# Kernel tuning notes

Hardware: AMD Instinct MI355X
Metric: run time of the kernel (lower is better)

## Reference

```python
import jax, jax.numpy as jnp
import numpy as np


def _l2norm(x, eps=1e-6):
    return x / jnp.sqrt(jnp.sum(x * x, axis=-1, keepdims=True) + eps)


def setup_inputs() -> dict:
    key = jax.random.key(0)
    k1, k2, k3, k4 = jax.random.split(key, 4)
    b, h, L, dk, dv = 2, 8, 4096, 128, 128
    q = jax.random.normal(k1, (b, h, L, dk), jnp.float32)
    k = jax.random.normal(k2, (b, h, L, dk), jnp.float32)
    v = jax.random.normal(k3, (b, h, L, dv), jnp.float32)
    beta = jax.random.uniform(k4, (b, h, L), jnp.float32)  # sigmoid(b_proj) in module -> (0,1)
    return {"q": q, "k": k, "v": v, "beta": beta, "chunk_size": 32}


def _delta_rule_chunkwise(q, k, v, beta, chunk_size):
    b, h, L, dk = q.shape
    dv = v.shape[-1]
    c = chunk_size
    pad = (-L) % c
    if pad:
        q = jnp.pad(q, ((0, 0), (0, 0), (0, pad), (0, 0)))
        k = jnp.pad(k, ((0, 0), (0, 0), (0, pad), (0, 0)))
        v = jnp.pad(v, ((0, 0), (0, 0), (0, pad), (0, 0)))
        beta = jnp.pad(beta, ((0, 0), (0, 0), (0, pad)))
    Lp = L + pad
    n = Lp // c

    q = _l2norm(q)
    k = _l2norm(k)
    v = v * beta[..., None]
    kb = k * beta[..., None]

    # (b,h,n,c,d)
    resh = lambda t: t.reshape(b, h, n, c, t.shape[-1])
    q, k, v, kb = resh(q), resh(k), resh(v), resh(kb)

    tri = jnp.triu(jnp.ones((c, c), bool), 0)        # upper incl diag
    tri_s = jnp.triu(jnp.ones((c, c), bool), 1)      # strict upper

    # forward substitution: inv = (I + strictly-lower(k_beta k^T))^{-1}-style recurrence
    inv = -jnp.einsum('bhncd,bhned->bhnce', kb, k)
    inv = jnp.where(tri, 0.0, inv)
    for i in range(1, c):  # fixed small chunk_size loop (c=32)
        upd = jnp.einsum('bhnk,bhnkj->bhnj', inv[..., i, :], inv[..., :, :i])
        inv = inv.at[..., i, :i].add(upd)
    inv = inv + jnp.eye(c, dtype=inv.dtype)

    u = inv @ v    # (b,h,n,c,dv)
    w = inv @ kb   # (b,h,n,c,dk)

    # chunk-recurrent state scan over the n blocks
    qs = jnp.moveaxis(q, 2, 0)
    ks = jnp.moveaxis(k, 2, 0)
    us = jnp.moveaxis(u, 2, 0)
    ws = jnp.moveaxis(w, 2, 0)
    S0 = jnp.zeros((b, h, dk, dv), q.dtype)

    def step(S, blk):
        q_i, k_i, u_i, w_i = blk
        attn = jnp.einsum('bhcd,bhed->bhce', q_i, k_i)
        attn = jnp.where(tri_s, 0.0, attn)                       # causal within chunk
        u_i = u_i - jnp.einsum('bhcd,bhde->bhce', w_i, S)
        o_i = jnp.einsum('bhcd,bhde->bhce', q_i, S) + jnp.einsum('bhce,bhed->bhcd', attn, u_i)
        S = S + jnp.einsum('bhcd,bhce->bhde', k_i, u_i)
        return S, o_i

    S, out = jax.lax.scan(step, S0, (qs, ks, us, ws))
    out = jnp.moveaxis(out, 0, 2).reshape(b, h, Lp, dv)[:, :, :L]
    return out, S


def reference(q, k, v, beta, chunk_size):
    return _delta_rule_chunkwise(q, k, v, beta, int(chunk_size))
```

## Files before the change

kernel.cpp:

```cpp
#include <hip/hip_runtime.h>
#include <cstddef>

#define BH   16
#define LSEQ 4096
#define DK   128
#define DV   128
#define C    32
#define NCH  128
#define DVB  16
#define NDVB 8
#define PP   136
#define PC   40
#define PS   136
#define AP   33

#define RECSZ 22528
#define OQ    0
#define OWH   4096
#define OWL   8192
#define OKTH  12288
#define OKTL  16384
#define OATH  20480
#define OATL  21504

typedef __attribute__((ext_vector_type(4))) float f32x4;
typedef __attribute__((ext_vector_type(8))) short short8;
typedef __attribute__((ext_vector_type(4))) short s16x4;

__device__ inline unsigned split_bf16(float x) {
    unsigned u = __builtin_bit_cast(unsigned, x);
    unsigned r = u + 0x7fffu + ((u >> 16) & 1u);
    unsigned h = r >> 16;
    float hf = __builtin_bit_cast(float, r & 0xffff0000u);
    float res = x - hf;
    unsigned u2 = __builtin_bit_cast(unsigned, res);
    unsigned r2 = u2 + 0x7fffu + ((u2 >> 16) & 1u);
    return (h << 16) | (r2 >> 16);
}
__device__ inline short hi_bf16(float x) {
    unsigned u = __builtin_bit_cast(unsigned, x);
    return (short)((u + 0x7fffu + ((u >> 16) & 1u)) >> 16);
}
__device__ inline short trunc_bf16(float x) {
    return (short)(__builtin_bit_cast(unsigned, x) >> 16);
}

__device__ inline short8 fld(const short* P, int row0, int pitch, int k0, int lane) {
    return *(const short8*)(P + (row0 + (lane & 15)) * pitch + k0 + ((lane >> 4) << 3));
}
__device__ inline short8 fldz128(const short* P, int row0, int ks, int lane) {
    int row = row0 + (lane & 15);
    int c = ks * 4 + (lane >> 4);
    return *(const short8*)(P + row * 128 + ((c ^ (row & 7)) << 3));
}
__device__ inline short8 fldz32(const short* P, int row0, int lane) {
    int row = row0 + (lane & 15);
    int c = lane >> 4;
    return *(const short8*)(P + row * 32 + ((c ^ (row & 3)) << 3));
}
__device__ inline f32x4 mf(short8 a, short8 b, f32x4 c) {
    return __builtin_amdgcn_mfma_f32_16x16x32_bf16(a, b, c, 0, 0, 0);
}
__device__ inline void build_ifrags(int lane, short8& Iev, short8& Iod) {
    int n = lane & 15, q = lane >> 4;
#pragma unroll
    for (int j = 0; j < 8; ++j) {
        Iev[j] = (q * 8 + j == n)      ? (short)0x3F80 : (short)0;
        Iod[j] = (q * 8 + j == n + 16) ? (short)0x3F80 : (short)0;
    }
}
__device__ inline void store8_z128(short* Pg, int row, int col0, s16x4 v) {
    int c = col0 >> 3;
    *(s16x4*)(Pg + row * 128 + ((c ^ (row & 7)) << 3) + (col0 & 7)) = v;
}
__device__ inline void store8_z32(short* Pg, int row, int col0, s16x4 v) {
    int c = col0 >> 3;
    *(s16x4*)(Pg + row * 32 + ((c ^ (row & 3)) << 3) + (col0 & 7)) = v;
}
__device__ inline void dma1k(const short* g, short* l, int lane) {
    __builtin_amdgcn_global_load_lds(
        (const __attribute__((address_space(1))) unsigned int*)(g + lane * 8),
        (__attribute__((address_space(3))) unsigned int*)l, 16, 0, 0);
}
__device__ inline void bar_lgkm() {
    asm volatile("s_waitcnt lgkmcnt(0)" ::: "memory");
    __builtin_amdgcn_s_barrier();
    asm volatile("" ::: "memory");
}

__global__ __launch_bounds__(256) void k_prep(const float* __restrict__ Q,
                                              const float* __restrict__ K,
                                              const float* __restrict__ V,
                                              const float* __restrict__ Beta,
                                              short* __restrict__ RECg,
                                              float* __restrict__ Uws) {
    __shared__ short knh[C * PP], knl[C * PP], vh[C * PP], vl[C * PP], qh[C * PP];
    __shared__ short knTh[DK * PC], knTl[DK * PC], vTh[DK * PC], vTl[DK * PC];
    __shared__ short Th[C * PC], Tl[C * PC];
    __shared__ float A[C * AP];
    __shared__ float sbeta[C];

    const int t = threadIdx.x, lane = t & 63, wv = t >> 6;
    const int quad = (t >> 4) & 3, l15 = t & 15;
    const int g = blockIdx.x;
    const size_t base = (size_t)g * (C * DK);
    short* rec = RECg + (size_t)g * RECSZ;
    short8 Iev, Iod;
    build_ifrags(lane, Iev, Iod);

    if (t < C) sbeta[t] = Beta[(size_t)(g >> 7) * LSEQ + (size_t)(g & 127) * C + t];

    const int sr = t >> 3, sc = (t & 7) * 16;
    f32x4 kk[4], vv[4], qq[4];
#pragma unroll
    for (int g4 = 0; g4 < 4; ++g4) {
        kk[g4] = *(const f32x4*)(K + base + 16 * t + 4 * g4);
        vv[g4] = *(const f32x4*)(V + base + 16 * t + 4 * g4);
        qq[g4] = *(const f32x4*)(Q + base + 16 * t + 4 * g4);
    }
    float ssk = 0.f, ssq = 0.f;
#pragma unroll
    for (int g4 = 0; g4 < 4; ++g4) {
#pragma unroll
        for (int e = 0; e < 4; ++e) {
            ssk += kk[g4][e] * kk[g4][e];
            ssq += qq[g4][e] * qq[g4][e];
        }
    }
    ssk += __shfl_xor(ssk, 1); ssk += __shfl_xor(ssk, 2); ssk += __shfl_xor(ssk, 4);
    ssq += __shfl_xor(ssq, 1); ssq += __shfl_xor(ssq, 2); ssq += __shfl_xor(ssq, 4);
    const float rk = rsqrtf(ssk + 1e-6f), rq = rsqrtf(ssq + 1e-6f);
#pragma unroll
    for (int half = 0; half < 2; ++half) {
        short8 h8, l8;
#pragma unroll
        for (int e = 0; e < 8; ++e) {
            unsigned p = split_bf16(kk[2 * half + (e >> 2)][e & 3] * rk);
            h8[e] = (short)(p >> 16); l8[e] = (short)(p & 0xffffu);
        }
        *(short8*)(knh + sr * PP + sc + 8 * half) = h8;
        *(short8*)(knl + sr * PP + sc + 8 * half) = l8;
#pragma unroll
        for (int e = 0; e < 8; ++e) {
            unsigned p = split_bf16(vv[2 * half + (e >> 2)][e & 3]);
            h8[e] = (short)(p >> 16); l8[e] = (short)(p & 0xffffu);
        }
        *(short8*)(vh + sr * PP + sc + 8 * half) = h8;
        *(short8*)(vl + sr * PP + sc + 8 * half) = l8;
        short8 q8;
#pragma unroll
        for (int e = 0; e < 8; ++e) q8[e] = hi_bf16(qq[2 * half + (e >> 2)][e & 3] * rq);
        *(short8*)(qh + sr * PP + sc + 8 * half) = q8;
        int c = (sc >> 3) + half;
        *(short8*)(rec + OQ + sr * 128 + ((c ^ (sr & 7)) << 3)) = q8;
    }
    __syncthreads();

    if (wv < 3) {
        const int a0 = (wv == 0) ? 0 : 16;
        const int b0 = (wv == 2) ? 16 : 0;
        f32x4 acc = {0.f, 0.f, 0.f, 0.f};
#pragma unroll
        for (int ks = 0; ks < 4; ++ks) {
            short8 ah = fld(knh, a0, PP, ks * 32, lane);
            short8 al = fld(knl, a0, PP, ks * 32, lane);
            short8 bh_ = fld(knh, b0, PP, ks * 32, lane);
            short8 bl_ = fld(knl, b0, PP, ks * 32, lane);
            acc = mf(ah, bh_, mf(ah, bl_, mf(al, bh_, acc)));
        }
#pragma unroll
        for (int r = 0; r < 4; ++r) {
            int row = a0 + quad * 4 + r, col = b0 + l15;
            A[row * AP + col] = (row > col) ? -sbeta[row] * acc[r] : 0.f;
        }
        f32x4 at = {0.f, 0.f, 0.f, 0.f};
#pragma unroll
        for (int ks = 0; ks < 4; ++ks) {
            short8 kh_ = fld(knh, b0, PP, ks * 32, lane);
            short8 kl_ = fld(knl, b0, PP, ks * 32, lane);
            short8 qf = fld(qh, a0, PP, ks * 32, lane);
            at = mf(kh_, qf, mf(kl_, qf, at));
        }
        s16x4 h4, l4;
#pragma unroll
        for (int r = 0; r < 4; ++r) {
            int cj = b0 + quad * 4 + r, ci = a0 + l15;
            float v = (cj <= ci) ? at[r] : 0.f;
            unsigned p = split_bf16(v);
            h4[r] = (short)(p >> 16); l4[r] = (short)(p & 0xffffu);
        }
        store8_z32(rec + OATH, a0 + l15, b0 + quad * 4, h4);
        store8_z32(rec + OATL, a0 + l15, b0 + quad * 4, l4);
    } else {
#pragma unroll
        for (int r = 0; r < 4; ++r) A[l15 * AP + 16 + quad * 4 + r] = 0.f;
        s16x4 z = {0, 0, 0, 0};
        store8_z32(rec + OATH, l15, 16 + quad * 4, z);
        store8_z32(rec + OATL, l15, 16 + quad * 4, z);
    }
    __syncthreads();

    auto tplane = [&](const short* src, short* dst, short* gdst) {
#pragma unroll
        for (int c0 = 0; c0 <= 16; c0 += 16) {
#pragma unroll
            for (int ks = 0; ks < 4; ++ks) {
                short8 fr = fld(src, c0, PP, ks * 32, lane);
                f32x4 z = {0.f, 0.f, 0.f, 0.f};
                f32x4 cA = mf(fr, Iev, z);
                f32x4 cB = mf(fr, Iod, z);
                s16x4 sA, sB;
#pragma unroll
                for (int r = 0; r < 4; ++r) { sA[r] = trunc_bf16(cA[r]); sB[r] = trunc_bf16(cB[r]); }
                *(s16x4*)(dst + (ks * 32 + l15) * PC + c0 + quad * 4) = sA;
                *(s16x4*)(dst + (ks * 32 + 16 + l15) * PC + c0 + quad * 4) = sB;
                if (gdst) {
                    store8_z32(gdst, ks * 32 + l15, c0 + quad * 4, sA);
                    store8_z32(gdst, ks * 32 + 16 + l15, c0 + quad * 4, sB);
                }
            }
        }
    };
    if (wv == 0) {
        tplane(knh, knTh, rec + OKTH);
        tplane(vl, vTl, nullptr);
    } else if (wv == 1) {
        tplane(knl, knTl, rec + OKTL);
    } else if (wv == 2) {
        tplane(vh, vTh, nullptr);
    } else if (lane < C) {
        const int j = lane;
        for (int i = 1; i < C; ++i) {
            float upd = 0.f;
            for (int kk2 = 1; kk2 < i; ++kk2) upd += A[i * AP + kk2] * A[kk2 * AP + j];
            if (j < i) A[i * AP + j] += upd;
        }
    }
    __syncthreads();

    {
        int tr = t >> 3, tc = (t & 7) * 4;
        s16x4 h4, l4;
#pragma unroll
        for (int e = 0; e < 4; ++e) {
            int j = tc + e;
            float val = ((tr == j) ? 1.f : (tr > j ? A[tr * AP + j] : 0.f)) * sbeta[j];
            unsigned p = split_bf16(val);
            h4[e] = (short)(p >> 16); l4[e] = (short)(p & 0xffffu);
        }
        *(s16x4*)(Th + tr * PC + tc) = h4;
        *(s16x4*)(Tl + tr * PC + tc) = l4;
    }
    __syncthreads();

    {
        const int ci0 = (wv & 1) * 16;
        short8 bTh = fld(Th, ci0, PC, 0, lane);
        short8 bTl = fld(Tl, ci0, PC, 0, lane);
        if (wv < 2) {
#pragma unroll
            for (int tt = 0; tt < 8; ++tt) {
                short8 ah = fld(vTh, tt * 16, PC, 0, lane);
                short8 al = fld(vTl, tt * 16, PC, 0, lane);
                f32x4 z = {0.f, 0.f, 0.f, 0.f};
                f32x4 acc = mf(ah, bTh, mf(ah, bTl, mf(al, bTh, z)));
                *(f32x4*)(Uws + (size_t)g * 4096 + (size_t)(ci0 + l15) * DK + tt * 16 + quad * 4) = acc;
            }
        } else {
#pragma unroll
            for (int tt = 0; tt < 8; ++tt) {
                short8 ah = fld(knTh, tt * 16, PC, 0, lane);
                short8 al = fld(knTl, tt * 16, PC, 0, lane);
                f32x4 z = {0.f, 0.f, 0.f, 0.f};
                f32x4 acc = mf(ah, bTh, mf(ah, bTl, mf(al, bTh, z)));
                s16x4 h4, l4;
#pragma unroll
                for (int r = 0; r < 4; ++r) {
                    unsigned p = split_bf16(acc[r]);
                    h4[r] = (short)(p >> 16); l4[r] = (short)(p & 0xffffu);
                }
                store8_z128(rec + OWH, ci0 + l15, tt * 16 + quad * 4, h4);
                store8_z128(rec + OWL, ci0 + l15, tt * 16 + quad * 4, l4);
            }
        }
    }
}

__global__ __launch_bounds__(512, 1) void k_scan(const short* __restrict__ RECg,
                                                 const float* __restrict__ Uws,
                                                 float* __restrict__ Out,
                                                 float* __restrict__ Sout) {
    __shared__ __attribute__((aligned(16))) short bALL[2][RECSZ];
    __shared__ short STh[DVB * PS], STl[DVB * PS];
    __shared__ short uTh[DVB * PC], uTl[DVB * PC];
    __shared__ float oP[2][16][20];

    const int t = threadIdx.x, lane = t & 63, wv = t >> 6;
    const int quad = (t >> 4) & 3, l15 = t & 15;
    const int db = blockIdx.x >> 4, bhi = blockIdx.x & 15;
    const int vcol = db * DVB;
    const int r0 = (wv & 1) * 16;
    const int dk0 = wv * 16;
    const size_t gb = (size_t)bhi * NCH;

    f32x4 accS = {0.f, 0.f, 0.f, 0.f};
    f32x4 ocp = {0.f, 0.f, 0.f, 0.f};
    float pu[4] = {0.f, 0.f, 0.f, 0.f};

    auto dma_rng = [&](int cc, int s, int q0, int n) {
        const short* src = RECg + (size_t)(gb + cc) * RECSZ;
        short* dst = bALL[s];
#pragma unroll 8
        for (int k = 0; k < n; ++k)
            dma1k(src + (q0 + k) * 512, dst + (q0 + k) * 512, lane);
    };
    auto pref_u = [&](int cc) {
        if (wv < 2) {
            const size_t ub = (gb + cc) * 4096;
#pragma unroll
            for (int r = 0; r < 4; ++r)
                pu[r] = Uws[ub + (size_t)(r0 + quad * 4 + r) * DK + vcol + l15];
        }
    };

    for (int e = t; e < DVB * PS; e += 512) { STh[e] = 0; STl[e] = 0; }
    if (wv >= 4)      dma_rng(0, 0, 12 + (wv - 4) * 8, 8);
    else if (wv >= 2) dma_rng(0, 0, (wv - 2) * 6, 6);
    pref_u(0);
    __syncthreads();

    for (int cid = 0; cid < NCH; ++cid) {
        const int cur = cid & 1;
        const short* pC = bALL[cur];

        short8 kth = fldz32(pC + OKTH, dk0, lane);
        short8 ktl = fldz32(pC + OKTL, dk0, lane);
        short8 bah = {}, bal = {};

        if (wv >= 4) {
            if (cid + 1 < NCH) dma_rng(cid + 1, cur ^ 1, 12 + (wv - 4) * 8, 8);
        } else if (wv >= 2) {
            short8 pSh[4], pSl[4], pQf[4];
#pragma unroll
            for (int ks = 0; ks < 4; ++ks) {
                pSh[ks] = fld(STh, 0, PS, ks * 32, lane);
                pSl[ks] = fld(STl, 0, PS, ks * 32, lane);
                pQf[ks] = fldz128(pC + OQ, r0, ks, lane);
            }
            if (cid + 1 < NCH) dma_rng(cid + 1, cur ^ 1, (wv - 2) * 6, 6);
            f32x4 z = {0.f, 0.f, 0.f, 0.f};
            f32x4 oa = mf(pSh[0], pQf[0], z), ob_ = mf(pSl[0], pQf[0], z);
            f32x4 oc2 = mf(pSh[1], pQf[1], z), od = mf(pSl[1], pQf[1], z);
            oa = mf(pSh[2], pQf[2], oa); ob_ = mf(pSl[2], pQf[2], ob_);
            oc2 = mf(pSh[3], pQf[3], oc2); od = mf(pSl[3], pQf[3], od);
            f32x4 osum = (oa + ob_) + (oc2 + od);
            *(f32x4*)(&oP[wv - 2][l15][quad * 4]) = osum;
        } else {
            if (cid > 0) {
                const size_t ob = ((size_t)bhi * LSEQ + (size_t)(cid - 1) * C) * DK;
                *(f32x4*)(Out + ob + (size_t)(r0 + l15) * DK + vcol + quad * 4) = ocp;
            }
            float p0 = pu[0], p1 = pu[1], p2 = pu[2], p3 = pu[3];
            if (cid + 1 < NCH) pref_u(cid + 1);

            f32x4 u0 = {-p0, -p1, -p2, -p3};
            f32x4 u1 = {0.f, 0.f, 0.f, 0.f}, u2 = {0.f, 0.f, 0.f, 0.f};
#pragma unroll
            for (int ks = 0; ks < 4; ++ks) {
                short8 wh_ = fldz128(pC + OWH, r0, ks, lane);
                short8 wl_ = fldz128(pC + OWL, r0, ks, lane);
                short8 sh_ = fld(STh, 0, PS, ks * 32, lane);
                short8 sl_ = fld(STl, 0, PS, ks * 32, lane);
                u0 = mf(wh_, sh_, u0);
                u1 = mf(wh_, sl_, u1);
                u2 = mf(wl_, sh_, u2);
            }
            f32x4 us = u0 + u1 + u2;
            s16x4 h4, l4;
#pragma unroll
            for (int r = 0; r < 4; ++r) {
                unsigned p = split_bf16(-us[r]);
                h4[r] = (short)(p >> 16); l4[r] = (short)(p & 0xffffu);
            }
            *(s16x4*)(uTh + l15 * PC + r0 + quad * 4) = h4;
            *(s16x4*)(uTl + l15 * PC + r0 + quad * 4) = l4;
            bah = fldz32(pC + OATH, r0, lane);
            bal = fldz32(pC + OATL, r0, lane);
        }
        bar_lgkm();

        short8 buh = fld(uTh, 0, PC, 0, lane);
        short8 bul = fld(uTl, 0, PC, 0, lane);
        if (wv < 2) {
            f32x4 oc = *(const f32x4*)(&oP[wv][l15][quad * 4]);
            f32x4 z = {0.f, 0.f, 0.f, 0.f};
            f32x4 m1 = mf(bul, bah, z);
            f32x4 m2 = mf(buh, bal, z);
            oc = mf(buh, bah, oc);
            ocp = oc + m1 + m2;
        }
        {
            f32x4 z = {0.f, 0.f, 0.f, 0.f};
            f32x4 ta = mf(ktl, buh, z);
            f32x4 tb = mf(kth, bul, z);
            accS = mf(kth, buh, accS);
            accS += ta + tb;
            s16x4 h4, l4;
#pragma unroll
            for (int r = 0; r < 4; ++r) {
                unsigned p = split_bf16(accS[r]);
                h4[r] = (short)(p >> 16); l4[r] = (short)(p & 0xffffu);
            }
            *(s16x4*)(STh + l15 * PS + dk0 + quad * 4) = h4;
            *(s16x4*)(STl + l15 * PS + dk0 + quad * 4) = l4;
        }
        if (wv >= 2) asm volatile("s_waitcnt vmcnt(0)" ::: "memory");
        bar_lgkm();
    }

    if (wv < 2) {
        const size_t ob = ((size_t)bhi * LSEQ + (size_t)(NCH - 1) * C) * DK;
        *(f32x4*)(Out + ob + (size_t)(r0 + l15) * DK + vcol + quad * 4) = ocp;
    }

#pragma unroll
    for (int r = 0; r < 4; ++r)
        Sout[(size_t)bhi * DK * DV + (size_t)(dk0 + quad * 4 + r) * DV + vcol + l15] = accS[r];
}

extern "C" void kernel_launch(void* const* d_in, const int* in_sizes, int n_in,
                              void* d_out, int out_size, void* d_ws, size_t ws_size,
                              hipStream_t stream) {
    const float* Q    = (const float*)d_in[0];
    const float* K    = (const float*)d_in[1];
    const float* V    = (const float*)d_in[2];
    const float* Beta = (const float*)d_in[3];

    float* Out  = (float*)d_out;
    float* Sout = Out + (size_t)BH * LSEQ * DV;

    short* RECg = (short*)d_ws;
    float* Uws  = (float*)(RECg + (size_t)BH * NCH * RECSZ);

    hipLaunchKernelGGL(k_prep, dim3(BH * NCH), dim3(256), 0, stream,
                       Q, K, V, Beta, RECg, Uws);
    hipLaunchKernelGGL(k_scan, dim3(BH * NDVB), dim3(512), 0, stream,
                       RECg, Uws, Out, Sout);
}
```

Baseline: 344.3 us.

## Load scan operands directly from global into registers instead of LDS DMA

The scan kernel no longer stages each chunk record into double-buffered LDS through global_load_lds. Each wave now loads its own W, Q, K^T and attention fragments straight from global memory into registers, prefetched one chunk ahead using a ping-pong pair of register sets, with the loop unrolled by two. The output-correction matmul moves to waves 2-3, which write Out directly. This drops the oP shared buffer and the extra vmcnt wait. The cost is higher register pressure and global load latency exposed on the serial chunk chain.

```diff
diff --git a/kernel.cpp b/kernel.cpp
--- a/kernel.cpp
+++ b/kernel.cpp
@@ -76,11 +76,6 @@
 __device__ inline void store8_z32(short* Pg, int row, int col0, s16x4 v) {
     int c = col0 >> 3;
     *(s16x4*)(Pg + row * 32 + ((c ^ (row & 3)) << 3) + (col0 & 7)) = v;
-}
-__device__ inline void dma1k(const short* g, short* l, int lane) {
-    __builtin_amdgcn_global_load_lds(
-        (const __attribute__((address_space(1))) unsigned int*)(g + lane * 8),
-        (__attribute__((address_space(3))) unsigned int*)l, 16, 0, 0);
 }
 __device__ inline void bar_lgkm() {
     asm volatile("s_waitcnt lgkmcnt(0)" ::: "memory");
@@ -290,10 +285,8 @@
                                                  const float* __restrict__ Uws,
                                                  float* __restrict__ Out,
                                                  float* __restrict__ Sout) {
-    __shared__ __attribute__((aligned(16))) short bALL[2][RECSZ];
     __shared__ short STh[DVB * PS], STl[DVB * PS];
     __shared__ short uTh[DVB * PC], uTl[DVB * PC];
-    __shared__ float oP[2][16][20];
 
     const int t = threadIdx.x, lane = t & 63, wv = t >> 6;
     const int quad = (t >> 4) & 3, l15 = t & 15;
@@ -304,15 +297,46 @@
     const size_t gb = (size_t)bhi * NCH;
 
     f32x4 accS = {0.f, 0.f, 0.f, 0.f};
-    f32x4 ocp = {0.f, 0.f, 0.f, 0.f};
     float pu[4] = {0.f, 0.f, 0.f, 0.f};
-
-    auto dma_rng = [&](int cc, int s, int q0, int n) {
-        const short* src = RECg + (size_t)(gb + cc) * RECSZ;
-        short* dst = bALL[s];
-#pragma unroll 8
-        for (int k = 0; k < n; ++k)
-            dma1k(src + (q0 + k) * 512, dst + (q0 + k) * 512, lane);
+    short8 kth = {}, ktl = {}, bah = {}, bal = {};
+
+    auto rec = [&](int cc) { return RECg + (size_t)(gb + cc) * RECSZ; };
+    auto gld128 = [&](const short* P, int row0, int ks) {
+        int row = row0 + l15;
+        int c = ks * 4 + (lane >> 4);
+        return *(const short8*)(P + row * 128 + ((c ^ (row & 7)) << 3));
+    };
+    auto gld32 = [&](const short* P, int row0) {
+        int row = row0 + l15;
+        int c = lane >> 4;
+        return *(const short8*)(P + row * 32 + ((c ^ (row & 3)) << 3));
+    };
+
+    struct EFrag { short8 a[4]; short8 b[4]; };
+    EFrag E0 = {}, E1 = {};
+
+    auto loadE = [&](int cc, EFrag& E) {
+        const short* rc = rec(cc);
+        if (wv < 2) {
+#pragma unroll
+            for (int ks = 0; ks < 4; ++ks) {
+                E.a[ks] = gld128(rc + OWH, r0, ks);
+                E.b[ks] = gld128(rc + OWL, r0, ks);
+            }
+        } else if (wv < 4) {
+#pragma unroll
+            for (int ks = 0; ks < 4; ++ks)
+                E.a[ks] = gld128(rc + OQ, r0, ks);
+        }
+    };
+    auto loadL = [&](int cc) {
+        const short* rc = rec(cc);
+        kth = gld32(rc + OKTH, dk0);
+        ktl = gld32(rc + OKTL, dk0);
+        if (wv >= 2 && wv < 4) {
+            bah = gld32(rc + OATH, r0);
+            bal = gld32(rc + OATL, r0);
+        }
     };
     auto pref_u = [&](int cc) {
         if (wv < 2) {
@@ -324,56 +348,27 @@
     };
 
     for (int e = t; e < DVB * PS; e += 512) { STh[e] = 0; STl[e] = 0; }
-    if (wv >= 4)      dma_rng(0, 0, 12 + (wv - 4) * 8, 8);
-    else if (wv >= 2) dma_rng(0, 0, (wv - 2) * 6, 6);
+    loadE(0, E0);
+    loadL(0);
     pref_u(0);
     __syncthreads();
 
-    for (int cid = 0; cid < NCH; ++cid) {
-        const int cur = cid & 1;
-        const short* pC = bALL[cur];
-
-        short8 kth = fldz32(pC + OKTH, dk0, lane);
-        short8 ktl = fldz32(pC + OKTL, dk0, lane);
-        short8 bah = {}, bal = {};
-
-        if (wv >= 4) {
-            if (cid + 1 < NCH) dma_rng(cid + 1, cur ^ 1, 12 + (wv - 4) * 8, 8);
-        } else if (wv >= 2) {
-            short8 pSh[4], pSl[4], pQf[4];
-#pragma unroll
-            for (int ks = 0; ks < 4; ++ks) {
-                pSh[ks] = fld(STh, 0, PS, ks * 32, lane);
-                pSl[ks] = fld(STl, 0, PS, ks * 32, lane);
-                pQf[ks] = fldz128(pC + OQ, r0, ks, lane);
-            }
-            if (cid + 1 < NCH) dma_rng(cid + 1, cur ^ 1, (wv - 2) * 6, 6);
-            f32x4 z = {0.f, 0.f, 0.f, 0.f};
-            f32x4 oa = mf(pSh[0], pQf[0], z), ob_ = mf(pSl[0], pQf[0], z);
-            f32x4 oc2 = mf(pSh[1], pQf[1], z), od = mf(pSl[1], pQf[1], z);
-            oa = mf(pSh[2], pQf[2], oa); ob_ = mf(pSl[2], pQf[2], ob_);
-            oc2 = mf(pSh[3], pQf[3], oc2); od = mf(pSl[3], pQf[3], od);
-            f32x4 osum = (oa + ob_) + (oc2 + od);
-            *(f32x4*)(&oP[wv - 2][l15][quad * 4]) = osum;
-        } else {
-            if (cid > 0) {
-                const size_t ob = ((size_t)bhi * LSEQ + (size_t)(cid - 1) * C) * DK;
-                *(f32x4*)(Out + ob + (size_t)(r0 + l15) * DK + vcol + quad * 4) = ocp;
-            }
+    auto body = [&](int cid, EFrag& EC, EFrag& EN) {
+        if (cid + 1 < NCH) loadE(cid + 1, EN);
+
+        f32x4 osum = {0.f, 0.f, 0.f, 0.f};
+        if (wv < 2) {
             float p0 = pu[0], p1 = pu[1], p2 = pu[2], p3 = pu[3];
             if (cid + 1 < NCH) pref_u(cid + 1);
-
             f32x4 u0 = {-p0, -p1, -p2, -p3};
             f32x4 u1 = {0.f, 0.f, 0.f, 0.f}, u2 = {0.f, 0.f, 0.f, 0.f};
 #pragma unroll
             for (int ks = 0; ks < 4; ++ks) {
-                short8 wh_ = fldz128(pC + OWH, r0, ks, lane);
-                short8 wl_ = fldz128(pC + OWL, r0, ks, lane);
                 short8 sh_ = fld(STh, 0, PS, ks * 32, lane);
                 short8 sl_ = fld(STl, 0, PS, ks * 32, lane);
-                u0 = mf(wh_, sh_, u0);
-                u1 = mf(wh_, sl_, u1);
-                u2 = mf(wl_, sh_, u2);
+                u0 = mf(EC.a[ks], sh_, u0);
+                u1 = mf(EC.a[ks], sl_, u1);
+                u2 = mf(EC.b[ks], sh_, u2);
             }
             f32x4 us = u0 + u1 + u2;
             s16x4 h4, l4;
@@ -384,20 +379,30 @@
             }
             *(s16x4*)(uTh + l15 * PC + r0 + quad * 4) = h4;
             *(s16x4*)(uTl + l15 * PC + r0 + quad * 4) = l4;
-            bah = fldz32(pC + OATH, r0, lane);
-            bal = fldz32(pC + OATL, r0, lane);
+        } else if (wv < 4) {
+            f32x4 z = {0.f, 0.f, 0.f, 0.f};
+            f32x4 oa = z, ob_ = z, oc2 = z, od = z;
+#pragma unroll
+            for (int ks = 0; ks < 4; ++ks) {
+                short8 pSh = fld(STh, 0, PS, ks * 32, lane);
+                short8 pSl = fld(STl, 0, PS, ks * 32, lane);
+                if (ks & 1) { oc2 = mf(pSh, EC.a[ks], oc2); od = mf(pSl, EC.a[ks], od); }
+                else        { oa  = mf(pSh, EC.a[ks], oa);  ob_ = mf(pSl, EC.a[ks], ob_); }
+            }
+            osum = (oa + ob_) + (oc2 + od);
         }
         bar_lgkm();
 
         short8 buh = fld(uTh, 0, PC, 0, lane);
         short8 bul = fld(uTl, 0, PC, 0, lane);
-        if (wv < 2) {
-            f32x4 oc = *(const f32x4*)(&oP[wv][l15][quad * 4]);
+        if (wv >= 2 && wv < 4) {
             f32x4 z = {0.f, 0.f, 0.f, 0.f};
             f32x4 m1 = mf(bul, bah, z);
             f32x4 m2 = mf(buh, bal, z);
-            oc = mf(buh, bah, oc);
-            ocp = oc + m1 + m2;
+            f32x4 oc = mf(buh, bah, osum);
+            oc = oc + m1 + m2;
+            const size_t ob = ((size_t)bhi * LSEQ + (size_t)cid * C) * DK;
+            *(f32x4*)(Out + ob + (size_t)(r0 + l15) * DK + vcol + quad * 4) = oc;
         }
         {
             f32x4 z = {0.f, 0.f, 0.f, 0.f};
@@ -414,13 +419,13 @@
             *(s16x4*)(STh + l15 * PS + dk0 + quad * 4) = h4;
             *(s16x4*)(STl + l15 * PS + dk0 + quad * 4) = l4;
         }
-        if (wv >= 2) asm volatile("s_waitcnt vmcnt(0)" ::: "memory");
+        if (cid + 1 < NCH) loadL(cid + 1);
         bar_lgkm();
-    }
-
-    if (wv < 2) {
-        const size_t ob = ((size_t)bhi * LSEQ + (size_t)(NCH - 1) * C) * DK;
-        *(f32x4*)(Out + ob + (size_t)(r0 + l15) * DK + vcol + quad * 4) = ocp;
+    };
+
+    for (int cp = 0; cp < NCH / 2; ++cp) {
+        body(2 * cp,     E0, E1);
+        body(2 * cp + 1, E1, E0);
     }
 
 #pragma unroll
```

Measured after the change: 454.5 us. 32.0% more time.
